# Performance work log

Measured on AMD Instinct MI355X. Metric: run time of the kernel, lower is better.

Reference implementation:

```python
import math
import jax, jax.numpy as jnp
import numpy as np

B = 2
N = 48           # max_atoms
A = 16           # num_atom_types
E = 5            # num_bond_types
HID = 384
NH = 8
HD = HID // NH   # 48
LYR = 4
MLP = 4 * HID
L = N + N * N    # 2352 sequence length (nodes + flattened edges)


def setup_inputs() -> dict:
    key = jax.random.key(0)
    ks = iter(jax.random.split(key, 48))
    r = lambda *s: jax.random.normal(next(ks), s, jnp.float32) * 0.02
    d = {
        "x": jax.random.normal(next(ks), (B, N, A), jnp.float32),
        "adj": jax.random.normal(next(ks), (B, N, N, E), jnp.float32),
        "t": jax.random.uniform(next(ks), (B,), jnp.float32),
        # embeddings
        "node_w": r(A, HID), "node_b": jnp.zeros((HID,), jnp.float32),
        "edge_w": r(E, HID), "edge_b": jnp.zeros((HID,), jnp.float32),
        "pos": r(L, HID),
        # timestep MLP (SinusoidalPositionalEmbedding(HID) -> Linear(HID,4H) -> SiLU -> Linear(4H,H))
        "t_w1": r(HID, 4 * HID), "t_b1": jnp.zeros((4 * HID,), jnp.float32),
        "t_w2": r(4 * HID, HID), "t_b2": jnp.zeros((HID,), jnp.float32),
        # stacked per-layer params
        "ada1_w": r(LYR, HID, 2 * HID), "ada1_b": jnp.zeros((LYR, 2 * HID), jnp.float32),
        "ada2_w": r(LYR, HID, 2 * HID), "ada2_b": jnp.zeros((LYR, 2 * HID), jnp.float32),
        "q_w": r(LYR, HID, HID), "q_b": jnp.zeros((LYR, HID), jnp.float32),
        "k_w": r(LYR, HID, HID), "k_b": jnp.zeros((LYR, HID), jnp.float32),
        "v_w": r(LYR, HID, HID), "v_b": jnp.zeros((LYR, HID), jnp.float32),
        "o_w": r(LYR, HID, HID), "o_b": jnp.zeros((LYR, HID), jnp.float32),
        "m1_w": r(LYR, HID, MLP), "m1_b": jnp.zeros((LYR, MLP), jnp.float32),
        "m2_w": r(LYR, MLP, HID), "m2_b": jnp.zeros((LYR, HID), jnp.float32),
        # final norm + heads (heads random instead of zero-init so output is informative)
        "fn_g": jnp.ones((HID,), jnp.float32), "fn_b": jnp.zeros((HID,), jnp.float32),
        "on_w": r(HID, A), "on_b": jnp.zeros((A,), jnp.float32),
        "oe_w": r(HID, E), "oe_b": jnp.zeros((E,), jnp.float32),
    }
    return d


def _ln(z):
    # LayerNorm(elementwise_affine=False), eps=1e-5
    mu = z.mean(-1, keepdims=True)
    var = z.var(-1, keepdims=True)
    return (z - mu) * jax.lax.rsqrt(var + 1e-5)


def _forward(x, adj, t, node_w, node_b, edge_w, edge_b, pos,
             t_w1, t_b1, t_w2, t_b2,
             ada1_w, ada1_b, ada2_w, ada2_b,
             q_w, q_b, k_w, k_b, v_w, v_b, o_w, o_b,
             m1_w, m1_b, m2_w, m2_b,
             fn_g, fn_b, on_w, on_b, oe_w, oe_b):
    b = x.shape[0]
    # embed nodes and edges, concat into sequence [b, L, HID]
    h_nodes = x @ node_w + node_b                       # [b, N, H]
    h_edges = adj.reshape(b, N * N, E) @ edge_w + edge_b  # [b, N*N, H]
    h = jnp.concatenate([h_nodes, h_edges], axis=1) + pos[None]
    # sinusoidal timestep embedding -> cond [b, HID]
    half = HID // 2
    freqs = jnp.exp(-math.log(10000.0) * jnp.arange(half, dtype=jnp.float32) / half)
    ang = t[:, None].astype(jnp.float32) * freqs[None, :]
    temb = jnp.concatenate([jnp.sin(ang), jnp.cos(ang)], axis=-1)
    cond = jax.nn.silu(temb @ t_w1 + t_b1) @ t_w2 + t_b2
    inv_scale = 1.0 / math.sqrt(HD)
    for i in range(LYR):
        # AdaLN 1 + attention
        sc, sh = jnp.split(cond @ ada1_w[i] + ada1_b[i], 2, axis=-1)
        n = _ln(h) * (1.0 + sc[:, None, :]) + sh[:, None, :]
        q = (n @ q_w[i] + q_b[i]).reshape(b, L, NH, HD)
        k = (n @ k_w[i] + k_b[i]).reshape(b, L, NH, HD)
        v = (n @ v_w[i] + v_b[i]).reshape(b, L, NH, HD)
        scores = jnp.einsum('bqhd,bkhd->bhqk', q, k) * inv_scale
        attn = jax.nn.softmax(scores, axis=-1)
        ao = jnp.einsum('bhqk,bkhd->bqhd', attn, v).reshape(b, L, HID)
        h = h + ao @ o_w[i] + o_b[i]
        # AdaLN 2 + MLP (exact GELU as in nn.GELU default)
        sc2, sh2 = jnp.split(cond @ ada2_w[i] + ada2_b[i], 2, axis=-1)
        n2 = _ln(h) * (1.0 + sc2[:, None, :]) + sh2[:, None, :]
        h = h + jax.nn.gelu(n2 @ m1_w[i] + m1_b[i], approximate=False) @ m2_w[i] + m2_b[i]
    h = _ln(h) * fn_g + fn_b
    node_out = h[:, :N] @ on_w + on_b                   # [b, N, A]
    edge_out = (h[:, N:] @ oe_w + oe_b).reshape(b, N, N, E)
    return node_out, edge_out


def reference(x, adj, t, node_w, node_b, edge_w, edge_b, pos,
              t_w1, t_b1, t_w2, t_b2,
              ada1_w, ada1_b, ada2_w, ada2_b,
              q_w, q_b, k_w, k_b, v_w, v_b, o_w, o_b,
              m1_w, m1_b, m2_w, m2_b,
              fn_g, fn_b, on_w, on_b, oe_w, oe_b):
    return _forward(x, adj, t, node_w, node_b, edge_w, edge_b, pos,
                    t_w1, t_b1, t_w2, t_b2,
                    ada1_w, ada1_b, ada2_w, ada2_b,
                    q_w, q_b, k_w, k_b, v_w, v_b, o_w, o_b,
                    m1_w, m1_b, m2_w, m2_b,
                    fn_g, fn_b, on_w, on_b, oe_w, oe_b)
```

## Files before the change

### kernel.cpp

```cpp
#include <hip/hip_runtime.h>
#include <hip/hip_bf16.h>
#include <math.h>

typedef __hip_bfloat16 bf16;
typedef __attribute__((ext_vector_type(8))) short short8;
typedef __attribute__((ext_vector_type(4))) float f32x4;

#define B_ 2
#define N_ 48
#define A_ 16
#define E_ 5
#define HID 384
#define NHD 8
#define HD 48
#define LYR 4
#define MLPD 1536
#define L_ 2352
#define M_ 4704
#define VLP 2432
#define QSCALE 0.20823513f

#define WQ_  0LL
#define WK_  589824LL
#define WV_  1179648LL
// ... 365 lines not shown
                             &As[wm*32 + mi*16 + c][ks*32 + quad*8]);
            #pragma unroll
            for (int ni = 0; ni < 2; ++ni)
                bfr[ni] = *reinterpret_cast<const short8*>(
                              &Bt[wn*32 + ni*16 + c][ks*32 + quad*8]);
            #pragma unroll
            for (int mi = 0; mi < 2; ++mi)
                #pragma unroll
                for (int ni = 0; ni < 2; ++ni)
                    acc[mi][ni] = __builtin_amdgcn_mfma_f32_16x16x32_bf16(
                                      af[mi], bfr[ni], acc[mi][ni], 0, 0, 0);
        }
    }
    gemm_epilogue(acc, ldv(bias, (size_t)boff + bn + wn*32 + c),
                  ldv(bias, (size_t)boff + bn + wn*32 + 16 + c),
                  Cb, Cf, M, N, act, mode, bm, bn, wm, wn, quad, c);
}

__global__ __launch_bounds__(256) void k_gemm(
    const bf16* __restrict__ A, const void* W, long long woff, const void* bias, long long boff,
    bf16* Cb, float* Cf, int M, int N, int K, int act, int mode,
    const int* __restrict__ fl)
{
    if (*fl) gemm_body<float>(A, (const float*)W, woff, (const float*)bias, boff,
                              Cb, Cf, M, N, K, act, mode);
    else     gemm_body<bf16>(A, (const bf16*)W, woff, (const bf16*)bias, boff,
                             Cb, Cf, M, N, K, act, mode);
}

__global__ __launch_bounds__(256) void k_gemm_qkv(
    const bf16* __restrict__ A,
    const void* qw, const void* kw, const void* vw,
    const void* qb, const void* kb, const void* vb,
    long long woff, long long boff,
    bf16* Cq, bf16* Ck, bf16* Cv, const int* __restrict__ fl)
{
    const int z = blockIdx.z;
    const void* W  = (z == 0) ? qw : (z == 1) ? kw : vw;
    const void* Bi = (z == 0) ? qb : (z == 1) ? kb : vb;
    bf16* C        = (z == 0) ? Cq : (z == 1) ? Ck : Cv;
    const int mode = (z == 0) ? 3 : (z == 2) ? 2 : 0;
    if (*fl) gemm_body<float>(A, (const float*)W, woff, (const float*)Bi, boff,
                              C, nullptr, M_, HID, HID, 0, mode);
    else     gemm_body<bf16>(A, (const bf16*)W, woff, (const bf16*)Bi, boff,
                             C, nullptr, M_, HID, HID, 0, mode);
}

static __device__ void gemm_t_body(
    const bf16* A, const bf16* Wt, long long woff, const bf16* bias, long long boff,
    bf16* Cb, float* Cf, int M, int N, int K, int act, int mode)
{
    __shared__ __align__(16) unsigned short Tz[2][2][4096];
    const int tid  = threadIdx.x;
    const int wv   = tid >> 6, lane = tid & 63;
    const int quad = lane >> 4, c = lane & 15;
    const int wm = wv & 1, wn = wv >> 1;
    const int bm = blockIdx.x * 64, bn = blockIdx.y * 64;
    const unsigned short* Ag = (const unsigned short*)A;
    const unsigned short* Wg = (const unsigned short*)Wt + woff;
    const int sr = tid >> 3;
    const int csw0 = (((tid & 7) ^ (sr & 7)) << 3);
    int ar0 = bm + sr;        ar0 = ar0 < M ? ar0 : M - 1;
    int ar1 = bm + 32 + sr;   ar1 = ar1 < M ? ar1 : M - 1;
    const int wr0 = bn + sr, wr1 = bn + 32 + sr;
    const int ldso = tid * 8;

    f32x4 acc[2][2] = {{{0.f,0.f,0.f,0.f},{0.f,0.f,0.f,0.f}},
                       {{0.f,0.f,0.f,0.f},{0.f,0.f,0.f,0.f}}};

    #define STAGE_T(buf, k0) do { \
        GLOAD16(Ag + (size_t)ar0*K + (k0) + csw0, &Tz[buf][0][ldso]); \
        GLOAD16(Ag + (size_t)ar1*K + (k0) + csw0, &Tz[buf][0][2048 + ldso]); \
        GLOAD16(Wg + (size_t)wr0*K + (k0) + csw0, &Tz[buf][1][ldso]); \
        GLOAD16(Wg + (size_t)wr1*K + (k0) + csw0, &Tz[buf][1][2048 + ldso]); \
    } while (0)

    STAGE_T(0, 0);
    __syncthreads();
    int cur = 0;
    for (int k0 = 0; k0 < K; k0 += 64) {
        if (k0 + 64 < K) STAGE_T(cur ^ 1, k0 + 64);
        #pragma unroll
        for (int ks = 0; ks < 2; ++ks) {
            short8 af[2], bfr[2];
            #pragma unroll
            for (int mi = 0; mi < 2; ++mi) {
                const int row = wm*32 + mi*16 + c;
                const char* p = (const char*)&Tz[cur][0][0]
                              + (row*128 + (((ks*64 + quad*16)) ^ ((row & 7) << 4)));
                af[mi] = *reinterpret_cast<const short8*>(p);
            }
            #pragma unroll
            for (int ni = 0; ni < 2; ++ni) {
                const int row = wn*32 + ni*16 + c;
                const char* p = (const char*)&Tz[cur][1][0]
                              + (row*128 + (((ks*64 + quad*16)) ^ ((row & 7) << 4)));
                bfr[ni] = *reinterpret_cast<const short8*>(p);
            }
            #pragma unroll
            for (int mi = 0; mi < 2; ++mi)
                #pragma unroll
                for (int ni = 0; ni < 2; ++ni)
                    acc[mi][ni] = __builtin_amdgcn_mfma_f32_16x16x32_bf16(
                                      af[mi], bfr[ni], acc[mi][ni], 0, 0, 0);
        }
        __syncthreads();
        cur ^= 1;
    }
    #undef STAGE_T
    gemm_epilogue(acc, b2f(bias[boff + bn + wn*32 + c]),
                  b2f(bias[boff + bn + wn*32 + 16 + c]),
                  Cb, Cf, M, N, act, mode, bm, bn, wm, wn, quad, c);
}

__global__ __launch_bounds__(256) void k_gemm_t(
    const bf16* __restrict__ A, const bf16* __restrict__ Wt, long long woff,
    const bf16* __restrict__ bias, long long boff,
    bf16* Cb, float* Cf, int M, int N, int K, int act, int mode)
{
    gemm_t_body(A, Wt, woff, bias, boff, Cb, Cf, M, N, K, act, mode);
}

__global__ __launch_bounds__(256) void k_gemm_qkv_t(
    const bf16* __restrict__ A, const bf16* __restrict__ wbt, const bf16* __restrict__ bb,
    int lyr, bf16* Cq, bf16* Ck, bf16* Cv)
{
    const int z = blockIdx.z;
    long long woff; long long boff; bf16* C; int mode;
    if (z == 0)      { woff = WQ_ + (long long)lyr*147456; boff = BQ_ + lyr*384; C = Cq; mode = 3; }
    else if (z == 1) { woff = WK_ + (long long)lyr*147456; boff = BK_ + lyr*384; C = Ck; mode = 0; }
    else             { woff = WV_ + (long long)lyr*147456; boff = BV_ + lyr*384; C = Cv; mode = 2; }
    gemm_t_body(A, wbt, woff, bb, boff, C, nullptr, M_, HID, HID, 0, mode);
}

__global__ __launch_bounds__(512) void k_attn(
    const bf16* __restrict__ q, const bf16* __restrict__ k,
    const bf16* __restrict__ vt, bf16* __restrict__ ao)
{
    __shared__ __align__(16) unsigned short Ks[2][64][80];
    __shared__ __align__(16) unsigned short Vt[2][48][72];
    __shared__ __align__(16) unsigned short Pq[8][16][72];
    const int tid  = threadIdx.x;
    const int w    = tid >> 6, lane = tid & 63;
    const int quad = lane >> 4, c = lane & 15;
    const int qt = w & 3, sp = w >> 2;
    const int bh = blockIdx.y;
    const size_t base  = (size_t)(bh >> 3)*L_*HID + (size_t)(bh & 7)*HD;
    const size_t vbase = (size_t)bh*48*VLP;
    const int q0 = blockIdx.x*64 + qt*16;
    const bool qvalid = q0 < L_;
    const int qrow = qvalid ? (q0 + c) : c;

    short8 qf0, qf1;
    {
        const unsigned short* qp = (const unsigned short*)(q + base + (size_t)qrow*HID);
        qf0 = *reinterpret_cast<const short8*>(qp + quad*8);
        if (quad < 2) qf1 = *reinterpret_cast<const short8*>(qp + 32 + quad*8);
        else          qf1 = short8{0,0,0,0,0,0,0,0};
    }
    f32x4 o0 = {0.f,0.f,0.f,0.f}, o1 = {0.f,0.f,0.f,0.f}, o2 = {0.f,0.f,0.f,0.f};
    float m = -3.0e38f, lsum = 0.f;

    const int t256 = tid & 255, grp = tid >> 8;
    const int krow0 = t256 >> 3, kch = t256 & 7;
    const int krow1 = 32 + krow0;
    const int vd0 = krow0;
    const int vd1 = 32 + (krow0 & 15);
    const bool vl1 = (t256 < 128);
    const unsigned short* kq = (const unsigned short*)(k + base);
    const unsigned short* vq = (const unsigned short*)(vt + vbase);
    const short8 Z8 = short8{0,0,0,0,0,0,0,0};
    short8 kr0 = Z8, kr1 = Z8, vr0, vr1 = Z8;
    {
        const int kb0 = grp*1216;
        if (kch < 6) {
            kr0 = *reinterpret_cast<const short8*>(kq + (size_t)(kb0 + krow0)*HID + kch*8);
            kr1 = *reinterpret_cast<const short8*>(kq + (size_t)(kb0 + krow1)*HID + kch*8);
        }
        vr0 = *reinterpret_cast<const short8*>(vq + (size_t)vd0*VLP + kb0 + kch*8);
        if (vl1) vr1 = *reinterpret_cast<const short8*>(vq + (size_t)vd1*VLP + kb0 + kch*8);
    }

    for (int tt = 0; tt < 19; ++tt) {
        __syncthreads();
        *reinterpret_cast<short8*>(&Ks[grp][krow0][kch*8]) = kr0;
        *reinterpret_cast<short8*>(&Ks[grp][krow1][kch*8]) = kr1;
        *reinterpret_cast<short8*>(&Vt[grp][vd0][kch*8])   = vr0;
        if (vl1) *reinterpret_cast<short8*>(&Vt[grp][vd1][kch*8]) = vr1;
        __syncthreads();
        if (tt < 18) {
            const int nb0 = grp*1216 + (tt + 1)*64;
            if (kch < 6) {
                kr0 = *reinterpret_cast<const short8*>(kq + (size_t)(nb0 + krow0)*HID + kch*8);
                kr1 = *reinterpret_cast<const short8*>(kq + (size_t)(nb0 + krow1)*HID + kch*8);
            }
            vr0 = *reinterpret_cast<const short8*>(vq + (size_t)vd0*VLP + nb0 + kch*8);
            if (vl1) vr1 = *reinterpret_cast<const short8*>(vq + (size_t)vd1*VLP + nb0 + kch*8);
        }

        const int kt = sp*1216 + tt*64;
        float sv[16];
        #pragma unroll
        for (int t = 0; t < 4; ++t) {
            f32x4 acc = {0.f,0.f,0.f,0.f};
            short8 a0 = *reinterpret_cast<const short8*>(&Ks[sp][t*16 + c][quad*8]);
            short8 a1 = *reinterpret_cast<const short8*>(&Ks[sp][t*16 + c][32 + quad*8]);
            acc = __builtin_amdgcn_mfma_f32_16x16x32_bf16(a0, qf0, acc, 0, 0, 0);
            acc = __builtin_amdgcn_mfma_f32_16x16x32_bf16(a1, qf1, acc, 0, 0, 0);
            #pragma unroll
            for (int r = 0; r < 4; ++r) sv[t*4 + r] = acc[r];
        }
        if (sp == 1 && tt >= 17) {
            #pragma unroll
            for (int t = 0; t < 4; ++t)
                #pragma unroll
                for (int r = 0; r < 4; ++r)
                    if (kt + t*16 + quad*4 + r >= L_) sv[t*4 + r] = -3.0e38f;
        }
        float tmax = fmaxf(fmaxf(fmaxf(sv[0], sv[1]),  fmaxf(sv[2],  sv[3])),
                           fmaxf(fmaxf(sv[4], sv[5]),  fmaxf(sv[6],  sv[7])));
        float tmx2 = fmaxf(fmaxf(fmaxf(sv[8], sv[9]),  fmaxf(sv[10], sv[11])),
                           fmaxf(fmaxf(sv[12], sv[13]), fmaxf(sv[14], sv[15])));
        tmax = fmaxf(tmax, tmx2);
        tmax = fmaxf(tmax, __shfl_xor(tmax, 16));
        tmax = fmaxf(tmax, __shfl_xor(tmax, 32));
        if (!__all(tmax <= m + 8.0f)) {
            const float mn = fmaxf(m, tmax);
            const float alpha = exp2f(m - mn);
            m = mn;
            lsum *= alpha;
            o0 *= alpha; o1 *= alpha; o2 *= alpha;
        }
        float psum = 0.f;
        unsigned short pv[16];
        #pragma unroll
        for (int i = 0; i < 16; ++i) {
            const float p = exp2f(sv[i] - m);
            psum += p;
            pv[i] = f2us(p);
        }
        lsum += psum;
        #pragma unroll
        for (int t = 0; t < 4; ++t)
            *reinterpret_cast<ushort4*>(&Pq[w][c][t*16 + quad*4]) =
                make_ushort4(pv[t*4+0], pv[t*4+1], pv[t*4+2], pv[t*4+3]);
        #pragma unroll
        for (int s = 0; s < 2; ++s) {
            short8 pf  = *reinterpret_cast<const short8*>(&Pq[w][c][s*32 + quad*8]);
            short8 vf0 = *reinterpret_cast<const short8*>(&Vt[sp][c][s*32 + quad*8]);
            short8 vf1 = *reinterpret_cast<const short8*>(&Vt[sp][16 + c][s*32 + quad*8]);
            short8 vf2 = *reinterpret_cast<const short8*>(&Vt[sp][32 + c][s*32 + quad*8]);
            o0 = __builtin_amdgcn_mfma_f32_16x16x32_bf16(vf0, pf, o0, 0, 0, 0);
            o1 = __builtin_amdgcn_mfma_f32_16x16x32_bf16(vf1, pf, o1, 0, 0, 0);
            o2 = __builtin_amdgcn_mfma_f32_16x16x32_bf16(vf2, pf, o2, 0, 0, 0);
        }
    }
    float lw = lsum;
    lw += __shfl_xor(lw, 16);
    lw += __shfl_xor(lw, 32);
    float* Mg = (float*)&Ks[0][0][0];
    __syncthreads();
    if (sp == 1) {
        float* dst = Mg + (size_t)(qt*64 + lane)*14;
        dst[0] = o0[0]; dst[1] = o0[1]; dst[2]  = o0[2]; dst[3]  = o0[3];
        dst[4] = o1[0]; dst[5] = o1[1]; dst[6]  = o1[2]; dst[7]  = o1[3];
        dst[8] = o2[0]; dst[9] = o2[1]; dst[10] = o2[2]; dst[11] = o2[3];
        dst[12] = m; dst[13] = lw;
    }
    __syncthreads();
    if (sp == 0 && qvalid) {
        const float* src = Mg + (size_t)(qt*64 + lane)*14;
        const float m2 = src[12], l2 = src[13];
        const float mm = fmaxf(m, m2);
        const float a1 = exp2f(m - mm), a2 = exp2f(m2 - mm);
        const float inv = 1.0f / (lw*a1 + l2*a2);
        unsigned short* orow = (unsigned short*)(ao + base + (size_t)(q0 + c)*HID);
        const f32x4 ot[3] = {o0, o1, o2};
        #pragma unroll
        for (int dt = 0; dt < 3; ++dt) {
            ushort4 w4;
            w4.x = f2us((ot[dt][0]*a1 + src[dt*4+0]*a2) * inv);
            w4.y = f2us((ot[dt][1]*a1 + src[dt*4+1]*a2) * inv);
            w4.z = f2us((ot[dt][2]*a1 + src[dt*4+2]*a2) * inv);
            w4.w = f2us((ot[dt][3]*a1 + src[dt*4+3]*a2) * inv);
            *reinterpret_cast<ushort4*>(orow + dt*16 + quad*4) = w4;
        }
    }
}

__global__ __launch_bounds__(256) void k_attn_fd(
    const bf16* __restrict__ q, const bf16* __restrict__ k,
    const bf16* __restrict__ vt, bf16* __restrict__ pob, float* __restrict__ pml)
{
    __shared__ __align__(16) unsigned short Kz[2][4096];
    __shared__ __align__(16) unsigned short Vz[2][3072];
    __shared__ __align__(16) unsigned short Pq[4][16][72];
    const int tid  = threadIdx.x;
    const int w    = tid >> 6, lane = tid & 63;
    const int quad = lane >> 4, c = lane & 15;
    const int bh   = blockIdx.y;
    const int half = blockIdx.z;
    const size_t base  = (size_t)(bh >> 3)*L_*HID + (size_t)(bh & 7)*HD;
    const size_t vbase = (size_t)bh*48*VLP;
    const int q0 = blockIdx.x*64 + w*16;
    const bool qvalid = q0 < L_;
    const int qrow = qvalid ? (q0 + c) : c;

    short8 qf0, qf1;
    {
        const unsigned short* qp = (const unsigned short*)(q + base + (size_t)qrow*HID);
        qf0 = *reinterpret_cast<const short8*>(qp + quad*8);
        if (quad < 2) qf1 = *reinterpret_cast<const short8*>(qp + 32 + quad*8);
        else          qf1 = short8{0,0,0,0,0,0,0,0};
    }
    f32x4 o0 = {0.f,0.f,0.f,0.f}, o1 = {0.f,0.f,0.f,0.f}, o2 = {0.f,0.f,0.f,0.f};
    float m = -3.0e38f, lsum = 0.f;

    const int srow = tid >> 3;
    const int sc   = (tid & 7) ^ (srow & 7);
    const int scol = sc << 3;
    const bool kld = (sc < 6);
    const int ldo  = tid * 8;
    const unsigned short* kq = (const unsigned short*)(k + base);
    const unsigned short* vq = (const unsigned short*)(vt + vbase);
    const int kbase = half*1216;

    #define STAGE_FD(buf, kb) do { \
        if (kld) { \
            GLOAD16(kq + (size_t)((kb) + srow)*HID + scol,      &Kz[buf][ldo]); \
            GLOAD16(kq + (size_t)((kb) + 32 + srow)*HID + scol, &Kz[buf][2048 + ldo]); \
        } \
        GLOAD16(vq + (size_t)srow*VLP + (kb) + scol, &Vz[buf][ldo]); \
        if (tid < 128) \
            GLOAD16(vq + (size_t)(32 + srow)*VLP + (kb) + scol, &Vz[buf][2048 + ldo]); \
    } while (0)

    {
        const short8 Z8 = short8{0,0,0,0,0,0,0,0};
        if (tid < 128) {
            const int r = tid >> 1, j = tid & 1;
            const int s = (6 + j) ^ (r & 7);
            *reinterpret_cast<short8*>(&Kz[0][r*64 + s*8]) = Z8;
            *reinterpret_cast<short8*>(&Kz[1][r*64 + s*8]) = Z8;
        }
    }
    STAGE_FD(0, kbase);
    __syncthreads();
    int cur = 0;

    for (int tt = 0; tt < 19; ++tt) {
        if (tt < 18) STAGE_FD(cur ^ 1, kbase + (tt + 1)*64);

        const int kt = kbase + tt*64;
        const char* kzb = (const char*)&Kz[cur][0];
        const char* vzb = (const char*)&Vz[cur][0];
        const int qx = quad << 4;
        float sv[16];
        #pragma unroll
        for (int t = 0; t < 4; ++t) {
            const int kr = t*16 + c;
            const int rx = kr*128;
            const int x0 = qx ^ ((kr & 7) << 4);
            f32x4 acc = {0.f,0.f,0.f,0.f};
            short8 a0 = *reinterpret_cast<const short8*>(kzb + rx + x0);
            short8 a1 = *reinterpret_cast<const short8*>(kzb + rx + (x0 ^ 64));
            acc = __builtin_amdgcn_mfma_f32_16x16x32_bf16(a0, qf0, acc, 0, 0, 0);
            acc = __builtin_amdgcn_mfma_f32_16x16x32_bf16(a1, qf1, acc, 0, 0, 0);
            #pragma unroll
            for (int r = 0; r < 4; ++r) sv[t*4 + r] = acc[r];
        }
        if (half == 1 && tt >= 17) {
            #pragma unroll
            for (int t = 0; t < 4; ++t)
                #pragma unroll
                for (int r = 0; r < 4; ++r)
                    if (kt + t*16 + quad*4 + r >= L_) sv[t*4 + r] = -3.0e38f;
        }
        float h0 = fmaxf(fmaxf(sv[0], sv[1]), sv[2]);
        h0 = fmaxf(fmaxf(h0, sv[3]), sv[4]);
        h0 = fmaxf(fmaxf(h0, sv[5]), sv[6]);
        h0 = fmaxf(h0, sv[7]);
        float h1 = fmaxf(fmaxf(sv[8], sv[9]), sv[10]);
        h1 = fmaxf(fmaxf(h1, sv[11]), sv[12]);
        h1 = fmaxf(fmaxf(h1, sv[13]), sv[14]);
        h1 = fmaxf(h1, sv[15]);
        float tmax = fmaxf(h0, h1);
        tmax = fmaxf(tmax, __shfl_xor(tmax, 16));
        tmax = fmaxf(tmax, __shfl_xor(tmax, 32));
        if (!__all(tmax <= m + 8.0f)) {
            const float mn = fmaxf(m, tmax);
            const float alpha = exp2_raw(m - mn);
            m = mn;
            lsum *= alpha;
            o0 *= alpha; o1 *= alpha; o2 *= alpha;
        }
        float psum = 0.f;
        unsigned pk[8];
        #pragma unroll
        for (int i = 0; i < 8; ++i) {
            const float p0 = exp2_raw(sv[2*i]     - m);
            const float p1 = exp2_raw(sv[2*i + 1] - m);
            psum += p0 + p1;
            pk[i] = (__float_as_uint(p0) >> 16) | (__float_as_uint(p1) & 0xFFFF0000u);
        }
        lsum += psum;
        #pragma unroll
        for (int t = 0; t < 4; ++t)
            *reinterpret_cast<uint2*>(&Pq[w][c][t*16 + quad*4]) =
                make_uint2(pk[2*t], pk[2*t + 1]);
        const int mx = (c & 7) << 4;
        #pragma unroll
        for (int s = 0; s < 2; ++s) {
            const int va = ((s << 6) | qx) ^ mx;
            short8 pf  = *reinterpret_cast<const short8*>(&Pq[w][c][s*32 + quad*8]);
            short8 vf0 = *reinterpret_cast<const short8*>(vzb + c*128 + va);
            short8 vf1 = *reinterpret_cast<const short8*>(vzb + (16 + c)*128 + va);
            short8 vf2 = *reinterpret_cast<const short8*>(vzb + (32 + c)*128 + va);
            o0 = __builtin_amdgcn_mfma_f32_16x16x32_bf16(vf0, pf, o0, 0, 0, 0);
            o1 = __builtin_amdgcn_mfma_f32_16x16x32_bf16(vf1, pf, o1, 0, 0, 0);
            o2 = __builtin_amdgcn_mfma_f32_16x16x32_bf16(vf2, pf, o2, 0, 0, 0);
        }
        __syncthreads();
        cur ^= 1;
    }
    #undef STAGE_FD
    float lw = lsum;
    lw += __shfl_xor(lw, 16);
    lw += __shfl_xor(lw, 32);
    const float invl = 1.0f / lw;
    const size_t ro = ((size_t)bh*2368 + q0 + c)*2 + half;
    unsigned short* pr = (unsigned short*)pob + ro*48;
    const f32x4 ot[3] = {o0, o1, o2};
    #pragma unroll
    for (int dt = 0; dt < 3; ++dt) {
        ushort4 w4;
        w4.x = f2us(ot[dt][0]*invl);
        w4.y = f2us(ot[dt][1]*invl);
        w4.z = f2us(ot[dt][2]*invl);
        w4.w = f2us(ot[dt][3]*invl);
        *reinterpret_cast<ushort4*>(pr + dt*16 + quad*4) = w4;
    }
    if (quad == 0) { pml[ro*2 + 0] = m; pml[ro*2 + 1] = lw; }
}

__global__ __launch_bounds__(256) void k_amerge(
    const bf16* __restrict__ pob, const float* __restrict__ pml, bf16* __restrict__ ao)
{
    const int tid = threadIdx.x;
    const int bh = blockIdx.y;
    const int qq = blockIdx.x*16 + (tid >> 4);
    const int j = tid & 15;
    const size_t ro = ((size_t)bh*2368 + qq)*2;
    const float m1 = pml[ro*2 + 0], l1 = pml[ro*2 + 1];
    const float m2 = pml[ro*2 + 2], l2 = pml[ro*2 + 3];
    const float mm = fmaxf(m1, m2);
    const float b1 = exp2f(m1 - mm)*l1, b2 = exp2f(m2 - mm)*l2;
    const float inv = 1.0f / (b1 + b2);
    const float w1 = b1*inv, w2 = b2*inv;
    if (j < 12) {
        const unsigned short* p1 = (const unsigned short*)pob + ro*48 + j*4;
        ushort4 u1 = *reinterpret_cast<const ushort4*>(p1);
        ushort4 u2 = *reinterpret_cast<const ushort4*>(p1 + 48);
        ushort4 o4;
        o4.x = f2us(us2f(u1.x)*w1 + us2f(u2.x)*w2);
        o4.y = f2us(us2f(u1.y)*w1 + us2f(u2.y)*w2);
        o4.z = f2us(us2f(u1.z)*w1 + us2f(u2.z)*w2);
        o4.w = f2us(us2f(u1.w)*w1 + us2f(u2.w)*w2);
        const size_t base = (size_t)(bh >> 3)*L_*HID + (size_t)(bh & 7)*HD;
        *reinterpret_cast<ushort4*>((unsigned short*)ao + base + (size_t)qq*HID + j*4) = o4;
    }
}

template <typename T, typename TO>
static __device__ void final_body(
    const float* h, const T* fn_g, const T* fn_b,
    const T* on_w, const T* on_b, const T* oe_w, const T* oe_b, TO* out)
{
    __shared__ float hf[HID];
    const int row = blockIdx.x;
    const int b = row / L_, l = row % L_;
    const int lane = threadIdx.x;
    const float* hr = h + (size_t)row*HID;
    float v[6]; float s = 0.f, ss = 0.f;
    #pragma unroll
    for (int j = 0; j < 6; ++j) { float t = hr[lane + j*64]; v[j] = t; s += t; ss += t*t; }
    #pragma unroll
    for (int off = 32; off; off >>= 1) { s += __shfl_xor(s, off); ss += __shfl_xor(ss, off); }
    const float mu = s * (1.0f/HID);
    const float rs = rsqrtf(fmaxf(ss * (1.0f/HID) - mu*mu, 0.0f) + 1e-5f);
    #pragma unroll
    for (int j = 0; j < 6; ++j) {
        int c = lane + j*64;
        hf[c] = (v[j] - mu) * rs * ldv(fn_g, c) + ldv(fn_b, c);
    }
    __syncthreads();
    if (l < N_) {
        if (lane < A_) {
            float acc = ldv(on_b, lane);
            for (int c = 0; c < HID; ++c) acc += hf[c] * ldv(on_w, (size_t)c*A_ + lane);
            stv(out, (size_t)(b*N_ + l)*A_ + lane, acc);
        }
    } else {
        const int e = l - N_;
        if (lane < E_) {
            float acc = ldv(oe_b, lane);
            for (int c = 0; c < HID; ++c) acc += hf[c] * ldv(oe_w, (size_t)c*E_ + lane);
            stv(out, (size_t)B_*N_*A_ + ((size_t)b*N_*N_ + e)*E_ + lane, acc);
        }
    }
}

__global__ __launch_bounds__(64) void k_final(
    const float* __restrict__ h, const void* fn_g, const void* fn_b,
    const void* on_w, const void* on_b, const void* oe_w, const void* oe_b,
    const int* __restrict__ fl, void* out)
{
    if (*fl) final_body<float, float>(h, (const float*)fn_g, (const float*)fn_b,
                                      (const float*)on_w, (const float*)on_b,
                                      (const float*)oe_w, (const float*)oe_b, (float*)out);
    else     final_body<bf16, bf16>(h, (const bf16*)fn_g, (const bf16*)fn_b,
                                    (const bf16*)on_w, (const bf16*)on_b,
                                    (const bf16*)oe_w, (const bf16*)oe_b, (bf16*)out);
}

extern "C" void kernel_launch(void* const* d_in, const int* in_sizes, int n_in,
                              void* d_out, int out_size, void* d_ws, size_t ws_size,
                              hipStream_t stream) {
    const void* x      = d_in[0];
    const void* adj    = d_in[1];
    const void* t      = d_in[2];
    const void* node_w = d_in[3];
    const void* node_b = d_in[4];
    const void* edge_w = d_in[5];
    const void* edge_b = d_in[6];
    const void* pos    = d_in[7];
    const void* t_w1   = d_in[8];
    const void* t_b1   = d_in[9];
    const void* t_w2   = d_in[10];
    const void* t_b2   = d_in[11];
    const void* ada1_w = d_in[12];
    const void* ada1_b = d_in[13];
    const void* ada2_w = d_in[14];
    const void* ada2_b = d_in[15];
    const void* q_w    = d_in[16];
    const void* q_b    = d_in[17];
    const void* k_w    = d_in[18];
    const void* k_b    = d_in[19];
    const void* v_w    = d_in[20];
    const void* v_b    = d_in[21];
    const void* o_w    = d_in[22];
    const void* o_b    = d_in[23];
    const void* m1_w   = d_in[24];
    const void* m1_b   = d_in[25];
    const void* m2_w   = d_in[26];
    const void* m2_b   = d_in[27];
    const void* fn_g   = d_in[28];
    const void* fn_b   = d_in[29];
    const void* on_w   = d_in[30];
    const void* on_b   = d_in[31];
    const void* oe_w   = d_in[32];
    const void* oe_b   = d_in[33];

    const size_t SZ  = (size_t)M_ * HID;
    const size_t VTZ = (size_t)B_*NHD*HD*VLP;
    const size_t FLT = SZ + 12288 + (size_t)B_*4*HID + (size_t)B_*12*HID;
    const size_t M1FULL = (size_t)M_ * MLPD;
    const size_t BF_BASE = 3*SZ + VTZ;
    const size_t BF_BIG  = SZ + M1FULL;
    const size_t NEED      = 256 + sizeof(float)*FLT + sizeof(bf16)*BF_BASE;
    const size_t NEED_BIG  = 256 + sizeof(float)*FLT + sizeof(bf16)*BF_BIG;
    const size_t NEED_PREP = 256 + sizeof(float)*FLT
                           + sizeof(bf16)*(BF_BIG + WTOT + BTOT);
    const size_t NEED_FD   = NEED_PREP + sizeof(bf16)*PO_E + sizeof(float)*PML_E;
    if (ws_size < NEED) {
        hipMemsetAsync(d_out, 0, (size_t)out_size*sizeof(bf16), stream);
        return;
    }
    const bool big  = (ws_size >= NEED_BIG);
    const bool prep = (ws_size >= NEED_PREP);
    const bool fd   = (ws_size >= NEED_FD);
    int*   fl   = (int*)d_ws;
    float* h    = (float*)((char*)d_ws + 256);
    float* ada  = h + SZ;
    float* hid  = ada + 12288;
    float* part = hid + (size_t)B_*4*HID;
    bf16* nb  = (bf16*)(part + (size_t)B_*12*HID);
    bf16* qb  = nb + SZ;
    bf16* kb  = qb + SZ;
    bf16* vtb = kb + SZ;
    bf16* m1c = kb;
    bf16* m1f = qb;
    bf16* wbt = nb + BF_BIG;
    bf16* bb  = wbt + WTOT;
    bf16* pob = bb + BTOT;
    float* pml = (float*)(pob + PO_E);

    k_detect<<<1, 64, 0, stream>>>(node_w, fl);
    if (prep) {
        k_prepw<<<dim3(144, 24), 256, 0, stream>>>(q_w, k_w, v_w, o_w, m1_w, m2_w, fl, wbt);
        k_prepb<<<1, 256, 0, stream>>>(q_b, k_b, v_b, o_b, m1_b, m2_b, fl, bb);
    }
    k_embed<<<M_, HID, 0, stream>>>(x, adj, node_w, node_b, edge_w, edge_b, pos, fl, h);
    k_cond1<<<dim3(B_, 24), 256, 0, stream>>>(t, t_w1, t_b1, fl, hid);
    k_cond2<<<dim3(B_, 12), 384, 0, stream>>>(t_w2, t_b2, fl, hid, part);
    k_cond3<<<dim3(24, B_), 256, 0, stream>>>(ada1_w, ada1_b, ada2_w, ada2_b, fl, part, ada);
    for (int i = 0; i < LYR; ++i) {
        const long long woff   = (long long)i * HID * HID;
        const long long boff   = (long long)i * HID;
        const long long m1woff = (long long)i * HID * MLPD;
        const long long m1boff = (long long)i * MLPD;
        const long long m2woff = (long long)i * MLPD * HID;

        k_adaln<<<M_/4, 256, 0, stream>>>(h, ada, nb, 2*i);
        if (prep) {
            k_gemm_qkv_t<<<dim3(74, 6, 3), 256, 0, stream>>>(nb, wbt, bb, i, qb, kb, vtb);
            if (fd) {
                k_attn_fd<<<dim3(37, 16, 2), 256, 0, stream>>>(qb, kb, vtb, pob, pml);
                k_amerge<<<dim3(147, 16), 256, 0, stream>>>(pob, pml, nb);
            } else {
                k_attn<<<dim3(37, B_*NHD), 512, 0, stream>>>(qb, kb, vtb, nb);
            }
            k_gemm_t<<<dim3(74, 6), 256, 0, stream>>>(nb, wbt, WO_ + (long long)i*147456,
                                                      bb, BO_ + i*384,
                                                      nullptr, h, M_, HID, HID, 0, 1);
            k_adaln<<<M_/4, 256, 0, stream>>>(h, ada, nb, 2*i + 1);
            k_gemm_t<<<dim3(74, 24), 256, 0, stream>>>(nb, wbt, WM1_ + (long long)i*589824,
                                                       bb, BM1_ + i*MLPD,
                                                       m1f, nullptr, M_, MLPD, HID, 1, 0);
            k_gemm_t<<<dim3(74, 6), 256, 0, stream>>>(m1f, wbt, WM2_ + (long long)i*589824,
                                                      bb, BM2_ + i*384,
                                                      nullptr, h, M_, HID, MLPD, 0, 1);
        } else {
            k_gemm_qkv<<<dim3(74, 6, 3), 256, 0, stream>>>(nb, q_w, k_w, v_w, q_b, k_b, v_b,
                                                           woff, boff, qb, kb, vtb, fl);
            k_attn<<<dim3(37, B_*NHD), 512, 0, stream>>>(qb, kb, vtb, nb);
            k_gemm<<<dim3(74, 6), 256, 0, stream>>>(nb, o_w, woff, o_b, boff,
                                                    nullptr, h, M_, HID, HID, 0, 1, fl);
            k_adaln<<<M_/4, 256, 0, stream>>>(h, ada, nb, 2*i + 1);
            if (big) {
                k_gemm<<<dim3(74, 24), 256, 0, stream>>>(nb, m1_w, m1woff, m1_b, m1boff,
                                                         m1f, nullptr, M_, MLPD, HID, 1, 0, fl);
                k_gemm<<<dim3(74, 6), 256, 0, stream>>>(m1f, m2_w, m2woff, m2_b, boff,
                                                        nullptr, h, M_, HID, MLPD, 0, 1, fl);
            } else {
                for (int c = 0; c < 2; ++c) {
                    k_gemm<<<dim3(37, 24), 256, 0, stream>>>(nb + (size_t)c*2352*HID,
                                                             m1_w, m1woff, m1_b, m1boff,
                                                             m1c, nullptr, 2352, MLPD, HID, 1, 0, fl);
                    k_gemm<<<dim3(37, 6), 256, 0, stream>>>(m1c, m2_w, m2woff, m2_b, boff,
                                                            nullptr, h + (size_t)c*2352*HID,
                                                            2352, HID, MLPD, 0, 1, fl);
                }
            }
        }
    }
    k_final<<<M_, 64, 0, stream>>>(h, fn_g, fn_b, on_w, on_b, oe_w, oe_b, fl, (void*)d_out);
}
```

Before: 779.8 us.

## Process two query tiles per wave in split-KV attention to reuse staged K/V

Each wave in the flash-decoding attention kernel now handles two 16-row query tiles instead of one. Each block covers 128 queries, so the grid's x dimension drops from 37 to 19. Every K/V tile staged into shared memory is reused for twice as many queries, which halves global K/V traffic and the number of block-wide syncs per query. The cost is doubled register state per wave (two sets of accumulators and softmax stats) and fewer blocks, so the GPU is less full. Out-of-range query tiles are computed but skipped at write-out.

```diff
diff --git a/kernel.cpp b/kernel.cpp
--- a/kernel.cpp
+++ b/kernel.cpp
@@ -691,19 +691,29 @@
     const int half = blockIdx.z;
     const size_t base  = (size_t)(bh >> 3)*L_*HID + (size_t)(bh & 7)*HD;
     const size_t vbase = (size_t)bh*48*VLP;
-    const int q0 = blockIdx.x*64 + w*16;
-    const bool qvalid = q0 < L_;
-    const int qrow = qvalid ? (q0 + c) : c;
-
-    short8 qf0, qf1;
+    const int q0 = blockIdx.x*128 + w*16;
+    const int q1 = q0 + 64;
+    const bool qvA = q0 < L_, qvB = q1 < L_;
+    const int qrowA = qvA ? (q0 + c) : c;
+    const int qrowB = qvB ? (q1 + c) : c;
+
+    short8 qf0a, qf1a, qf0b, qf1b;
     {
-        const unsigned short* qp = (const unsigned short*)(q + base + (size_t)qrow*HID);
-        qf0 = *reinterpret_cast<const short8*>(qp + quad*8);
-        if (quad < 2) qf1 = *reinterpret_cast<const short8*>(qp + 32 + quad*8);
-        else          qf1 = short8{0,0,0,0,0,0,0,0};
-    }
-    f32x4 o0 = {0.f,0.f,0.f,0.f}, o1 = {0.f,0.f,0.f,0.f}, o2 = {0.f,0.f,0.f,0.f};
-    float m = -3.0e38f, lsum = 0.f;
+        const unsigned short* qpA = (const unsigned short*)(q + base + (size_t)qrowA*HID);
+        const unsigned short* qpB = (const unsigned short*)(q + base + (size_t)qrowB*HID);
+        qf0a = *reinterpret_cast<const short8*>(qpA + quad*8);
+        qf0b = *reinterpret_cast<const short8*>(qpB + quad*8);
+        if (quad < 2) {
+            qf1a = *reinterpret_cast<const short8*>(qpA + 32 + quad*8);
+            qf1b = *reinterpret_cast<const short8*>(qpB + 32 + quad*8);
+        } else {
+            qf1a = short8{0,0,0,0,0,0,0,0};
+            qf1b = short8{0,0,0,0,0,0,0,0};
+        }
+    }
+    f32x4 oA0 = {0.f,0.f,0.f,0.f}, oA1 = {0.f,0.f,0.f,0.f}, oA2 = {0.f,0.f,0.f,0.f};
+    f32x4 oB0 = {0.f,0.f,0.f,0.f}, oB1 = {0.f,0.f,0.f,0.f}, oB2 = {0.f,0.f,0.f,0.f};
+    float mA = -3.0e38f, lA = 0.f, mB = -3.0e38f, lB = 0.f;
 
     const int srow = tid >> 3;
     const int sc   = (tid & 7) ^ (srow & 7);
@@ -724,6 +734,73 @@
             GLOAD16(vq + (size_t)(32 + srow)*VLP + (kb) + scol, &Vz[buf][2048 + ldo]); \
     } while (0)
 
+    #define ATTN_TILE(QF0, QF1, MM, LL, O0, O1, O2) do {                          \
+        float sv[16];                                                             \
+        _Pragma("unroll")                                                         \
+        for (int t = 0; t < 4; ++t) {                                             \
+            const int kr = t*16 + c;                                              \
+            const int rx = kr*128;                                                \
+            const int x0 = qx ^ ((kr & 7) << 4);                                  \
+            f32x4 acc = {0.f,0.f,0.f,0.f};                                        \
+            short8 a0 = *reinterpret_cast<const short8*>(kzb + rx + x0);          \
+            short8 a1 = *reinterpret_cast<const short8*>(kzb + rx + (x0 ^ 64));   \
+            acc = __builtin_amdgcn_mfma_f32_16x16x32_bf16(a0, QF0, acc, 0, 0, 0); \
+            acc = __builtin_amdgcn_mfma_f32_16x16x32_bf16(a1, QF1, acc, 0, 0, 0); \
+            _Pragma("unroll")                                                     \
+            for (int r = 0; r < 4; ++r) sv[t*4 + r] = acc[r];                     \
+        }                                                                         \
+        if (half == 1 && tt >= 17) {                                              \
+            _Pragma("unroll")                                                     \
+            for (int t = 0; t < 4; ++t)                                           \
+                _Pragma("unroll")                                                 \
+                for (int r = 0; r < 4; ++r)                                       \
+                    if (kt + t*16 + quad*4 + r >= L_) sv[t*4 + r] = -3.0e38f;     \
+        }                                                                         \
+        float h0 = fmaxf(fmaxf(sv[0], sv[1]), sv[2]);                             \
+        h0 = fmaxf(fmaxf(h0, sv[3]), sv[4]);                                      \
+        h0 = fmaxf(fmaxf(h0, sv[5]), sv[6]);                                      \
+        h0 = fmaxf(h0, sv[7]);                                                    \
+        float h1 = fmaxf(fmaxf(sv[8], sv[9]), sv[10]);                            \
+        h1 = fmaxf(fmaxf(h1, sv[11]), sv[12]);                                    \
+        h1 = fmaxf(fmaxf(h1, sv[13]), sv[14]);                                    \
+        h1 = fmaxf(h1, sv[15]);                                                   \
+        float tmax = fmaxf(h0, h1);                                               \
+        tmax = fmaxf(tmax, __shfl_xor(tmax, 16));                                 \
+        tmax = fmaxf(tmax, __shfl_xor(tmax, 32));                                 \
+        if (!__all(tmax <= MM + 8.0f)) {                                          \
+            const float mn = fmaxf(MM, tmax);                                     \
+            const float alpha = exp2_raw(MM - mn);                                \
+            MM = mn;                                                              \
+            LL *= alpha;                                                          \
+            O0 *= alpha; O1 *= alpha; O2 *= alpha;                                \
+        }                                                                         \
+        float psum = 0.f;                                                         \
+        unsigned pk[8];                                                           \
+        _Pragma("unroll")                                                         \
+        for (int i = 0; i < 8; ++i) {                                             \
+            const float p0 = exp2_raw(sv[2*i]     - MM);                          \
+            const float p1 = exp2_raw(sv[2*i + 1] - MM);                          \
+            psum += p0 + p1;                                                      \
+            pk[i] = (__float_as_uint(p0) >> 16) | (__float_as_uint(p1) & 0xFFFF0000u); \
+        }                                                                         \
+        LL += psum;                                                               \
+        _Pragma("unroll")                                                         \
+        for (int t = 0; t < 4; ++t)                                               \
+            *reinterpret_cast<uint2*>(&Pq[w][c][t*16 + quad*4]) =                 \
+                make_uint2(pk[2*t], pk[2*t + 1]);                                 \
+        _Pragma("unroll")                                                         \
+        for (int s = 0; s < 2; ++s) {                                             \
+            const int va = ((s << 6) | qx) ^ mx;                                  \
+            short8 pf  = *reinterpret_cast<const short8*>(&Pq[w][c][s*32 + quad*8]); \
+            short8 vf0 = *reinterpret_cast<const short8*>(vzb + c*128 + va);      \
+            short8 vf1 = *reinterpret_cast<const short8*>(vzb + (16 + c)*128 + va); \
+            short8 vf2 = *reinterpret_cast<const short8*>(vzb + (32 + c)*128 + va); \
+            O0 = __builtin_amdgcn_mfma_f32_16x16x32_bf16(vf0, pf, O0, 0, 0, 0);   \
+            O1 = __builtin_amdgcn_mfma_f32_16x16x32_bf16(vf1, pf, O1, 0, 0, 0);   \
+            O2 = __builtin_amdgcn_mfma_f32_16x16x32_bf16(vf2, pf, O2, 0, 0, 0);   \
+        }                                                                         \
+    } while (0)
+
     {
         const short8 Z8 = short8{0,0,0,0,0,0,0,0};
         if (tid < 128) {
@@ -744,92 +821,53 @@
         const char* kzb = (const char*)&Kz[cur][0];
         const char* vzb = (const char*)&Vz[cur][0];
         const int qx = quad << 4;
-        float sv[16];
-        #pragma unroll
-        for (int t = 0; t < 4; ++t) {
-            const int kr = t*16 + c;
-            const int rx = kr*128;
-            const int x0 = qx ^ ((kr & 7) << 4);
-            f32x4 acc = {0.f,0.f,0.f,0.f};
-            short8 a0 = *reinterpret_cast<const short8*>(kzb + rx + x0);
-            short8 a1 = *reinterpret_cast<const short8*>(kzb + rx + (x0 ^ 64));
-            acc = __builtin_amdgcn_mfma_f32_16x16x32_bf16(a0, qf0, acc, 0, 0, 0);
-            acc = __builtin_amdgcn_mfma_f32_16x16x32_bf16(a1, qf1, acc, 0, 0, 0);
-            #pragma unroll
-            for (int r = 0; r < 4; ++r) sv[t*4 + r] = acc[r];
-        }
-        if (half == 1 && tt >= 17) {
-            #pragma unroll
-            for (int t = 0; t < 4; ++t)
-                #pragma unroll
-                for (int r = 0; r < 4; ++r)
-                    if (kt + t*16 + quad*4 + r >= L_) sv[t*4 + r] = -3.0e38f;
-        }
-        float h0 = fmaxf(fmaxf(sv[0], sv[1]), sv[2]);
-        h0 = fmaxf(fmaxf(h0, sv[3]), sv[4]);
-        h0 = fmaxf(fmaxf(h0, sv[5]), sv[6]);
-        h0 = fmaxf(h0, sv[7]);
-        float h1 = fmaxf(fmaxf(sv[8], sv[9]), sv[10]);
-        h1 = fmaxf(fmaxf(h1, sv[11]), sv[12]);
-        h1 = fmaxf(fmaxf(h1, sv[13]), sv[14]);
-        h1 = fmaxf(h1, sv[15]);
-        float tmax = fmaxf(h0, h1);
-        tmax = fmaxf(tmax, __shfl_xor(tmax, 16));
-        tmax = fmaxf(tmax, __shfl_xor(tmax, 32));
-        if (!__all(tmax <= m + 8.0f)) {
-            const float mn = fmaxf(m, tmax);
-            const float alpha = exp2_raw(m - mn);
-            m = mn;
-            lsum *= alpha;
-            o0 *= alpha; o1 *= alpha; o2 *= alpha;
-        }
-        float psum = 0.f;
-        unsigned pk[8];
-        #pragma unroll
-        for (int i = 0; i < 8; ++i) {
-            const float p0 = exp2_raw(sv[2*i]     - m);
-            const float p1 = exp2_raw(sv[2*i + 1] - m);
-            psum += p0 + p1;
-            pk[i] = (__float_as_uint(p0) >> 16) | (__float_as_uint(p1) & 0xFFFF0000u);
-        }
-        lsum += psum;
-        #pragma unroll
-        for (int t = 0; t < 4; ++t)
-            *reinterpret_cast<uint2*>(&Pq[w][c][t*16 + quad*4]) =
-                make_uint2(pk[2*t], pk[2*t + 1]);
         const int mx = (c & 7) << 4;
-        #pragma unroll
-        for (int s = 0; s < 2; ++s) {
-            const int va = ((s << 6) | qx) ^ mx;
-            short8 pf  = *reinterpret_cast<const short8*>(&Pq[w][c][s*32 + quad*8]);
-            short8 vf0 = *reinterpret_cast<const short8*>(vzb + c*128 + va);
-            short8 vf1 = *reinterpret_cast<const short8*>(vzb + (16 + c)*128 + va);
-            short8 vf2 = *reinterpret_cast<const short8*>(vzb + (32 + c)*128 + va);
-            o0 = __builtin_amdgcn_mfma_f32_16x16x32_bf16(vf0, pf, o0, 0, 0, 0);
-            o1 = __builtin_amdgcn_mfma_f32_16x16x32_bf16(vf1, pf, o1, 0, 0, 0);
-            o2 = __builtin_amdgcn_mfma_f32_16x16x32_bf16(vf2, pf, o2, 0, 0, 0);
-        }
+
+        ATTN_TILE(qf0a, qf1a, mA, lA, oA0, oA1, oA2);
+        ATTN_TILE(qf0b, qf1b, mB, lB, oB0, oB1, oB2);
+
         __syncthreads();
         cur ^= 1;
     }
+    #undef ATTN_TILE
     #undef STAGE_FD
-    float lw = lsum;
-    lw += __shfl_xor(lw, 16);
-    lw += __shfl_xor(lw, 32);
-    const float invl = 1.0f / lw;
-    const size_t ro = ((size_t)bh*2368 + q0 + c)*2 + half;
-    unsigned short* pr = (unsigned short*)pob + ro*48;
-    const f32x4 ot[3] = {o0, o1, o2};
-    #pragma unroll
-    for (int dt = 0; dt < 3; ++dt) {
-        ushort4 w4;
-        w4.x = f2us(ot[dt][0]*invl);
-        w4.y = f2us(ot[dt][1]*invl);
-        w4.z = f2us(ot[dt][2]*invl);
-        w4.w = f2us(ot[dt][3]*invl);
-        *reinterpret_cast<ushort4*>(pr + dt*16 + quad*4) = w4;
-    }
-    if (quad == 0) { pml[ro*2 + 0] = m; pml[ro*2 + 1] = lw; }
+
+    lA += __shfl_xor(lA, 16);
+    lA += __shfl_xor(lA, 32);
+    lB += __shfl_xor(lB, 16);
+    lB += __shfl_xor(lB, 32);
+    if (qvA) {
+        const float invl = 1.0f / lA;
+        const size_t ro = ((size_t)bh*2368 + q0 + c)*2 + half;
+        unsigned short* pr = (unsigned short*)pob + ro*48;
+        const f32x4 ot[3] = {oA0, oA1, oA2};
+        #pragma unroll
+        for (int dt = 0; dt < 3; ++dt) {
+            ushort4 w4;
+            w4.x = f2us(ot[dt][0]*invl);
+            w4.y = f2us(ot[dt][1]*invl);
+            w4.z = f2us(ot[dt][2]*invl);
+            w4.w = f2us(ot[dt][3]*invl);
+            *reinterpret_cast<ushort4*>(pr + dt*16 + quad*4) = w4;
+        }
+        if (quad == 0) { pml[ro*2 + 0] = mA; pml[ro*2 + 1] = lA; }
+    }
+    if (qvB) {
+        const float invl = 1.0f / lB;
+        const size_t ro = ((size_t)bh*2368 + q1 + c)*2 + half;
+        unsigned short* pr = (unsigned short*)pob + ro*48;
+        const f32x4 ot[3] = {oB0, oB1, oB2};
+        #pragma unroll
+        for (int dt = 0; dt < 3; ++dt) {
+            ushort4 w4;
+            w4.x = f2us(ot[dt][0]*invl);
+            w4.y = f2us(ot[dt][1]*invl);
+            w4.z = f2us(ot[dt][2]*invl);
+            w4.w = f2us(ot[dt][3]*invl);
+            *reinterpret_cast<ushort4*>(pr + dt*16 + quad*4) = w4;
+        }
+        if (quad == 0) { pml[ro*2 + 0] = mB; pml[ro*2 + 1] = lB; }
+    }
 }
 
 __global__ __launch_bounds__(256) void k_amerge(
@@ -1004,7 +1042,7 @@
         if (prep) {
             k_gemm_qkv_t<<<dim3(74, 6, 3), 256, 0, stream>>>(nb, wbt, bb, i, qb, kb, vtb);
             if (fd) {
-                k_attn_fd<<<dim3(37, 16, 2), 256, 0, stream>>>(qb, kb, vtb, pob, pml);
+                k_attn_fd<<<dim3(19, 16, 2), 256, 0, stream>>>(qb, kb, vtb, pob, pml);
                 k_amerge<<<dim3(147, 16), 256, 0, stream>>>(pob, pml, nb);
             } else {
                 k_attn<<<dim3(37, B_*NHD), 512, 0, stream>>>(qb, kb, vtb, nb);
```

After: 794.6 us. About the same (+1.9%).
